# Optimization experiments

Hardware: AMD Instinct MI355X
Metric: run time of the kernel (lower is better)

Reference implementation:

```python
import jax, jax.numpy as jnp
import numpy as np
from math import comb

N_VARS = 6
DEGREE = 4
NUM_TERMS = 768
D1 = DEGREE + 1          # coeffs per variable row (input)
D2 = 2 * DEGREE + 1      # coeffs per variable row after squaring


def _bern_mul_weights(d):
    # Bernstein-basis product: c_k = sum_i C(d,i)C(d,k-i)/C(2d,k) a_i b_{k-i}
    W = np.zeros((d + 1, d + 1, 2 * d + 1), dtype=np.float32)
    for i in range(d + 1):
        for j in range(d + 1):
            W[i, j, i + j] = comb(d, i) * comb(d, j) / comb(2 * d, i + j)
    return W

_W_NP = _bern_mul_weights(DEGREE)          # (D1, D1, D2) product weights
_E_NP = _W_NP.sum(axis=1)                  # (D1, D2) degree elevation d -> 2d (multiply by ones poly)


def ibf_minmax(P):
    """Interval bounds of an implicit-Bernstein-form poly P: (T, V, D1).
    Per term: interval of each var row (Bernstein coeff min/max bound the poly on [0,1]),
    interval product across vars, then interval sum across terms."""
    lo = P.min(-1)  # (T, V)
    hi = P.max(-1)
    T = P.shape[0]
    ones = jnp.ones((T,), P.dtype)

    def step(carry, x):
        clo, chi = carry
        xlo, xhi = x
        cand = jnp.stack([clo * xlo, clo * xhi, chi * xlo, chi * xhi])
        return (cand.min(0), cand.max(0)), None

    (tlo, thi), _ = jax.lax.scan(step, (ones, ones), (lo.T, hi.T))  # scan over V vars
    return tlo.sum(), thi.sum()


def relu_coeffs_under(l, u):
    # quadratic lower relaxation of ReLU on [l,u]: q(x) = (x^2 - l x)/(u - l)
    den = jnp.where(u - l > 0, u - l, jnp.ones_like(u))
    quad = jnp.stack([1.0 / den, -l / den, jnp.zeros_like(l)])
    lin = jnp.array([0.0, 1.0, 0.0], dtype=quad.dtype)
    zero = jnp.zeros(3, dtype=quad.dtype)
    return jnp.where(l >= 0, lin, jnp.where(u <= 0, zero, quad))


def relu_coeffs_over(l, u):
    # quadratic upper relaxation: q(x) = u (x - l)^2 / (u - l)^2
    den = jnp.where(u - l > 0, u - l, jnp.ones_like(u))
    d2 = den * den
    quad = jnp.stack([u / d2, -2.0 * u * l / d2, u * l * l / d2])
    lin = jnp.array([0.0, 1.0, 0.0], dtype=quad.dtype)
    zero = jnp.zeros(3, dtype=quad.dtype)
    return jnp.where(l >= 0, lin, jnp.where(u <= 0, zero, quad))


def quad_of_poly(P, coeffs):
    """Compose quadratic a x^2 + b x + c with IBF poly P (T, V, D1).
    Returns IBF poly with T^2 + T + 1 terms, per-var degree 2*DEGREE."""
    a, b, c = coeffs[0], coeffs[1], coeffs[2]
    W = jnp.asarray(_W_NP)
    E = jnp.asarray(_E_NP)
    T, V, _ = P.shape
    # P^2: all pairwise term products; per-var Bernstein row product
    sq = jnp.einsum('tvi,svj,ijk->tsvk', P, P, W).reshape(T * T, V, D2)
    sq = sq.at[:, 0, :].multiply(a)          # scale by a on first var row
    # b * P: elevate each row from degree d to 2d, scale by b
    lin = jnp.einsum('tvi,ik->tvk', P, E)
    lin = lin.at[:, 0, :].multiply(b)
    # constant term c: all-ones rows, first row scaled by c
    const = jnp.ones((1, V, D2), P.dtype).at[0, 0, :].multiply(c)
    out = jnp.concatenate([sq, lin, const], axis=0)  # (T^2+T+1, V, D2)
    return out.reshape((T * T + T + 1) * V, D2)


def setup_inputs() -> dict:
    key = jax.random.key(0)
    k1, k2 = jax.random.split(key)
    input_under = jax.random.normal(k1, (NUM_TERMS * N_VARS, D1), dtype=jnp.float32)
    input_over = jax.random.normal(k2, (NUM_TERMS * N_VARS, D1), dtype=jnp.float32)
    return {"input_under": input_under, "input_over": input_over}


def reference(input_under, input_over):
    Pu = input_under.reshape(input_under.shape[0] // N_VARS, N_VARS, D1)
    Po = input_over.reshape(input_over.shape[0] // N_VARS, N_VARS, D1)
    l = ibf_minmax(Pu)[0]
    u = ibf_minmax(Po)[1]
    # torch.tensor([l, u]) detaches in the original -> stop_gradient for faithfulness
    l = jax.lax.stop_gradient(l)
    u = jax.lax.stop_gradient(u)
    cu = relu_coeffs_under(l, u)
    co = relu_coeffs_over(l, u)
    relu_node_under = quad_of_poly(Pu, cu)
    relu_node_over = quad_of_poly(Po, co)
    return relu_node_under, relu_node_over
```

## Files before the change

### kernel.cpp

```cpp
#include <hip/hip_runtime.h>

#define T_TERMS 768
#define NV 6
#define D1 5
#define D2 9
#define T2 (T_TERMS * T_TERMS)
#define PTOT (T2 + T_TERMS + 1)
#define NROWS ((unsigned int)PTOT * NV)
#define NOUT (NROWS * (unsigned int)D2)

typedef float f4 __attribute__((ext_vector_type(4)));

__global__ void bounds_kernel(const float* __restrict__ Pu,
                              const float* __restrict__ Po,
                              float* __restrict__ coef) {
    int t = threadIdx.x;
    float tlo = 0.f, thi = 0.f;
    if (t < T_TERMS) {
        float clo_u = 1.f, chi_u = 1.f;
        float clo_o = 1.f, chi_o = 1.f;
        const float* pu = Pu + t * NV * D1;
        const float* po = Po + t * NV * D1;
        #pragma unroll
        for (int v = 0; v < NV; ++v) {
            float lo = pu[v * 5 + 0], hi = lo;
            #pragma unroll
            for (int i = 1; i < 5; ++i) {
                float x = pu[v * 5 + i];
                lo = fminf(lo, x); hi = fmaxf(hi, x);
            }
            float a = clo_u * lo, b = clo_u * hi, c = chi_u * lo, d = chi_u * hi;
            clo_u = fminf(fminf(a, b), fminf(c, d));
            chi_u = fmaxf(fmaxf(a, b), fmaxf(c, d));
            lo = po[v * 5 + 0]; hi = lo;
            #pragma unroll
            for (int i = 1; i < 5; ++i) {
                float x = po[v * 5 + i];
                lo = fminf(lo, x); hi = fmaxf(hi, x);
            }
            a = clo_o * lo; b = clo_o * hi; c = chi_o * lo; d = chi_o * hi;
            clo_o = fminf(fminf(a, b), fminf(c, d));
            chi_o = fmaxf(fmaxf(a, b), fmaxf(c, d));
        }
        tlo = clo_u;
        thi = chi_o;
    }
    __shared__ float slo[12], shi[12];
    for (int off = 32; off; off >>= 1) {
        tlo += __shfl_down(tlo, off);
        thi += __shfl_down(thi, off);
    }
    int wave = threadIdx.x >> 6;
    if ((threadIdx.x & 63) == 0) { slo[wave] = tlo; shi[wave] = thi; }
    __syncthreads();
    if (threadIdx.x == 0) {
        float l = 0.f, u = 0.f;
        #pragma unroll
        for (int w = 0; w < 12; ++w) { l += slo[w]; u += shi[w]; }
        float den = (u - l > 0.f) ? (u - l) : 1.f;
        float au, bu, cu, ao, bo, co;
        if (l >= 0.f) {
            au = 0.f; bu = 1.f; cu = 0.f;
            ao = 0.f; bo = 1.f; co = 0.f;
        } else if (u <= 0.f) {
            au = bu = cu = 0.f;
            ao = bo = co = 0.f;
        } else {
            au = 1.f / den; bu = -l / den; cu = 0.f;
            float d2 = den * den;
            ao = u / d2; bo = -2.f * u * l / d2; co = u * l * l / d2;
        }
        coef[0] = au; coef[1] = bu; coef[2] = cu;
        coef[3] = ao; coef[4] = bo; coef[5] = co;
    }
}

__global__ __launch_bounds__(256) void expand_kernel(
        const float* __restrict__ Pu,
        const float* __restrict__ Po,
        const float* __restrict__ coef,
        float* __restrict__ out) {
    __shared__ float lds[256 * D2];
    static constexpr float Wt[5][5] = {
        {1.0f,        4.0f/8.0f,   6.0f/28.0f,  4.0f/56.0f,  1.0f/70.0f},
        {4.0f/8.0f,   16.0f/28.0f, 24.0f/56.0f, 16.0f/70.0f, 4.0f/56.0f},
        {6.0f/28.0f,  24.0f/56.0f, 36.0f/70.0f, 24.0f/56.0f, 6.0f/28.0f},
        {4.0f/56.0f,  16.0f/70.0f, 24.0f/56.0f, 16.0f/28.0f, 4.0f/8.0f},
        {1.0f/70.0f,  4.0f/56.0f,  6.0f/28.0f,  4.0f/8.0f,   1.0f}
    };

    const unsigned tid = threadIdx.x;
    const unsigned bid = blockIdx.x;
    const unsigned ten = blockIdx.y;
    const float* __restrict__ P = ten ? Po : Pu;
    const float* __restrict__ c3 = coef + ten * 3;

    const unsigned rr = bid * 256u + tid;
    const unsigned nvalid = min(256u, NROWS - bid * 256u);

    float c[9] = {0.f,0.f,0.f,0.f,0.f,0.f,0.f,0.f,0.f};
    if (rr < NROWS) {
        unsigned p = rr / 6u;
        unsigned v = rr - p * 6u;
        float a[5], b[5];
        float scale = 1.f;
        if (p < (unsigned)T2) {
            unsigned t = p / (unsigned)T_TERMS;
            unsigned s = p - t * (unsigned)T_TERMS;
            const float* A = P + (t * NV + v) * D1;
            const float* B = P + (s * NV + v) * D1;
            #pragma unroll
            for (int i = 0; i < 5; ++i) { a[i] = A[i]; b[i] = B[i]; }
            if (v == 0u) scale = c3[0];
        } else if (p < (unsigned)(T2 + T_TERMS)) {
            unsigned t = p - (unsigned)T2;
            const float* A = P + (t * NV + v) * D1;
            #pragma unroll
            for (int i = 0; i < 5; ++i) { a[i] = A[i]; b[i] = 1.f; }
            if (v == 0u) scale = c3[1];
        } else {
            #pragma unroll
            for (int i = 0; i < 5; ++i) { a[i] = 1.f; b[i] = 1.f; }
            if (v == 0u) scale = c3[2];
        }
        #pragma unroll
        for (int i = 0; i < 5; ++i) a[i] *= scale;
        #pragma unroll
        for (int i = 0; i < 5; ++i)
            #pragma unroll
            for (int j = 0; j < 5; ++j)
                c[i + j] = fmaf(Wt[i][j] * a[i], b[j], c[i + j]);
    }
    #pragma unroll
    for (int k = 0; k < 9; ++k) lds[tid * 9u + k] = c[k];
    __syncthreads();

    float* __restrict__ o = out + (size_t)ten * NOUT + (size_t)bid * (256u * D2);
    const unsigned nd = nvalid * 9u;
    if (nvalid == 256u) {
        const f4* l4 = (const f4*)lds;
        f4* o4 = (f4*)o;
        __builtin_nontemporal_store(l4[tid], o4 + tid);
        __builtin_nontemporal_store(l4[tid + 256u], o4 + tid + 256u);
        if (tid < 64u)
            __builtin_nontemporal_store(l4[tid + 512u], o4 + tid + 512u);
    } else {
        for (unsigned x = tid; x < nd; x += 256u)
            __builtin_nontemporal_store(lds[x], o + x);
    }
}

extern "C" void kernel_launch(void* const* d_in, const int* in_sizes, int n_in,
                              void* d_out, int out_size, void* d_ws, size_t ws_size,
                              hipStream_t stream) {
    const float* Pu = (const float*)d_in[0];
    const float* Po = (const float*)d_in[1];
    float* coef = (float*)d_ws;
    float* out = (float*)d_out;

    bounds_kernel<<<1, 768, 0, stream>>>(Pu, Po, coef);

    unsigned int blocks_x = (NROWS + 255u) / 256u;
    dim3 grid(blocks_x, 2, 1);
    expand_kernel<<<grid, 256, 0, stream>>>(Pu, Po, coef, out);
}
```

Measured before the change: 268.9 us.

## Split bounds across two blocks, vectorize loads, use regular stores

The bounds reduction now runs as two blocks, one per tensor, with float2 register loads, and a separate single-thread kernel computes the relaxation coefficients. The expand kernel loads each 5-coefficient row as an unaligned float4 plus a scalar, and it replaces the nontemporal output stores with ordinary vector stores. The aim is a shorter serial prologue and cheaper input loads. The cost is an extra kernel launch, and the output writes may now pass through cache differently.

```diff
diff --git a/kernel.cpp b/kernel.cpp
--- a/kernel.cpp
+++ b/kernel.cpp
@@ -10,69 +10,67 @@
 #define NOUT (NROWS * (unsigned int)D2)
 
 typedef float f4 __attribute__((ext_vector_type(4)));
+typedef float f4u __attribute__((ext_vector_type(4), aligned(4)));
+typedef float f2 __attribute__((ext_vector_type(2)));
 
 __global__ void bounds_kernel(const float* __restrict__ Pu,
                               const float* __restrict__ Po,
-                              float* __restrict__ coef) {
+                              float* __restrict__ ws) {
+    const float* __restrict__ P = blockIdx.x ? Po : Pu;
     int t = threadIdx.x;
-    float tlo = 0.f, thi = 0.f;
+    float acc = 0.f;
     if (t < T_TERMS) {
-        float clo_u = 1.f, chi_u = 1.f;
-        float clo_o = 1.f, chi_o = 1.f;
-        const float* pu = Pu + t * NV * D1;
-        const float* po = Po + t * NV * D1;
+        f2 r[15];
+        const f2* p2 = (const f2*)(P + t * (NV * D1));
+        #pragma unroll
+        for (int i = 0; i < 15; ++i) r[i] = p2[i];
+        const float* rf = (const float*)r;
+        float clo = 1.f, chi = 1.f;
         #pragma unroll
         for (int v = 0; v < NV; ++v) {
-            float lo = pu[v * 5 + 0], hi = lo;
+            float lo = rf[v * 5 + 0], hi = lo;
             #pragma unroll
             for (int i = 1; i < 5; ++i) {
-                float x = pu[v * 5 + i];
+                float x = rf[v * 5 + i];
                 lo = fminf(lo, x); hi = fmaxf(hi, x);
             }
-            float a = clo_u * lo, b = clo_u * hi, c = chi_u * lo, d = chi_u * hi;
-            clo_u = fminf(fminf(a, b), fminf(c, d));
-            chi_u = fmaxf(fmaxf(a, b), fmaxf(c, d));
-            lo = po[v * 5 + 0]; hi = lo;
-            #pragma unroll
-            for (int i = 1; i < 5; ++i) {
-                float x = po[v * 5 + i];
-                lo = fminf(lo, x); hi = fmaxf(hi, x);
-            }
-            a = clo_o * lo; b = clo_o * hi; c = chi_o * lo; d = chi_o * hi;
-            clo_o = fminf(fminf(a, b), fminf(c, d));
-            chi_o = fmaxf(fmaxf(a, b), fmaxf(c, d));
+            float a = clo * lo, b = clo * hi, c = chi * lo, d = chi * hi;
+            clo = fminf(fminf(a, b), fminf(c, d));
+            chi = fmaxf(fmaxf(a, b), fmaxf(c, d));
         }
-        tlo = clo_u;
-        thi = chi_o;
+        acc = blockIdx.x ? chi : clo;
     }
-    __shared__ float slo[12], shi[12];
-    for (int off = 32; off; off >>= 1) {
-        tlo += __shfl_down(tlo, off);
-        thi += __shfl_down(thi, off);
-    }
+    __shared__ float sred[12];
+    for (int off = 32; off; off >>= 1) acc += __shfl_down(acc, off);
     int wave = threadIdx.x >> 6;
-    if ((threadIdx.x & 63) == 0) { slo[wave] = tlo; shi[wave] = thi; }
+    if ((threadIdx.x & 63) == 0) sred[wave] = acc;
     __syncthreads();
     if (threadIdx.x == 0) {
-        float l = 0.f, u = 0.f;
+        float s = 0.f;
         #pragma unroll
-        for (int w = 0; w < 12; ++w) { l += slo[w]; u += shi[w]; }
-        float den = (u - l > 0.f) ? (u - l) : 1.f;
-        float au, bu, cu, ao, bo, co;
-        if (l >= 0.f) {
-            au = 0.f; bu = 1.f; cu = 0.f;
-            ao = 0.f; bo = 1.f; co = 0.f;
-        } else if (u <= 0.f) {
-            au = bu = cu = 0.f;
-            ao = bo = co = 0.f;
-        } else {
-            au = 1.f / den; bu = -l / den; cu = 0.f;
-            float d2 = den * den;
-            ao = u / d2; bo = -2.f * u * l / d2; co = u * l * l / d2;
-        }
-        coef[0] = au; coef[1] = bu; coef[2] = cu;
-        coef[3] = ao; coef[4] = bo; coef[5] = co;
+        for (int w = 0; w < 12; ++w) s += sred[w];
+        ws[blockIdx.x] = s;
     }
+}
+
+__global__ void coef_kernel(float* __restrict__ ws) {
+    float l = ws[0], u = ws[1];
+    float den = (u - l > 0.f) ? (u - l) : 1.f;
+    float au, bu, cu, ao, bo, co;
+    if (l >= 0.f) {
+        au = 0.f; bu = 1.f; cu = 0.f;
+        ao = 0.f; bo = 1.f; co = 0.f;
+    } else if (u <= 0.f) {
+        au = bu = cu = 0.f;
+        ao = bo = co = 0.f;
+    } else {
+        au = 1.f / den; bu = -l / den; cu = 0.f;
+        float d2 = den * den;
+        ao = u / d2; bo = -2.f * u * l / d2; co = u * l * l / d2;
+    }
+    float* coef = ws + 2;
+    coef[0] = au; coef[1] = bu; coef[2] = cu;
+    coef[3] = ao; coef[4] = bo; coef[5] = co;
 }
 
 __global__ __launch_bounds__(256) void expand_kernel(
@@ -102,29 +100,30 @@
     if (rr < NROWS) {
         unsigned p = rr / 6u;
         unsigned v = rr - p * 6u;
-        float a[5], b[5];
+        f4 a4; float a1;
+        f4 b4; float b1;
         float scale = 1.f;
         if (p < (unsigned)T2) {
             unsigned t = p / (unsigned)T_TERMS;
             unsigned s = p - t * (unsigned)T_TERMS;
             const float* A = P + (t * NV + v) * D1;
             const float* B = P + (s * NV + v) * D1;
-            #pragma unroll
-            for (int i = 0; i < 5; ++i) { a[i] = A[i]; b[i] = B[i]; }
+            a4 = *(const f4u*)A;  a1 = A[4];
+            b4 = *(const f4u*)B;  b1 = B[4];
             if (v == 0u) scale = c3[0];
         } else if (p < (unsigned)(T2 + T_TERMS)) {
             unsigned t = p - (unsigned)T2;
             const float* A = P + (t * NV + v) * D1;
-            #pragma unroll
-            for (int i = 0; i < 5; ++i) { a[i] = A[i]; b[i] = 1.f; }
+            a4 = *(const f4u*)A;  a1 = A[4];
+            b4 = (f4){1.f,1.f,1.f,1.f};  b1 = 1.f;
             if (v == 0u) scale = c3[1];
         } else {
-            #pragma unroll
-            for (int i = 0; i < 5; ++i) { a[i] = 1.f; b[i] = 1.f; }
+            a4 = (f4){1.f,1.f,1.f,1.f};  a1 = 1.f;
+            b4 = (f4){1.f,1.f,1.f,1.f};  b1 = 1.f;
             if (v == 0u) scale = c3[2];
         }
-        #pragma unroll
-        for (int i = 0; i < 5; ++i) a[i] *= scale;
+        float a[5] = {a4.x * scale, a4.y * scale, a4.z * scale, a4.w * scale, a1 * scale};
+        float b[5] = {b4.x, b4.y, b4.z, b4.w, b1};
         #pragma unroll
         for (int i = 0; i < 5; ++i)
             #pragma unroll
@@ -136,17 +135,17 @@
     __syncthreads();
 
     float* __restrict__ o = out + (size_t)ten * NOUT + (size_t)bid * (256u * D2);
-    const unsigned nd = nvalid * 9u;
     if (nvalid == 256u) {
         const f4* l4 = (const f4*)lds;
         f4* o4 = (f4*)o;
-        __builtin_nontemporal_store(l4[tid], o4 + tid);
-        __builtin_nontemporal_store(l4[tid + 256u], o4 + tid + 256u);
+        o4[tid]         = l4[tid];
+        o4[tid + 256u]  = l4[tid + 256u];
         if (tid < 64u)
-            __builtin_nontemporal_store(l4[tid + 512u], o4 + tid + 512u);
+            o4[tid + 512u] = l4[tid + 512u];
     } else {
+        const unsigned nd = nvalid * 9u;
         for (unsigned x = tid; x < nd; x += 256u)
-            __builtin_nontemporal_store(lds[x], o + x);
+            o[x] = lds[x];
     }
 }
 
@@ -155,12 +154,13 @@
                               hipStream_t stream) {
     const float* Pu = (const float*)d_in[0];
     const float* Po = (const float*)d_in[1];
-    float* coef = (float*)d_ws;
+    float* ws = (float*)d_ws;
     float* out = (float*)d_out;
 
-    bounds_kernel<<<1, 768, 0, stream>>>(Pu, Po, coef);
+    bounds_kernel<<<2, 768, 0, stream>>>(Pu, Po, ws);
+    coef_kernel<<<1, 1, 0, stream>>>(ws);
 
     unsigned int blocks_x = (NROWS + 255u) / 256u;
     dim3 grid(blocks_x, 2, 1);
-    expand_kernel<<<grid, 256, 0, stream>>>(Pu, Po, coef, out);
+    expand_kernel<<<grid, 256, 0, stream>>>(Pu, Po, ws + 2, out);
 }
```

Result: faster. 253.3 us (-5.8%).
